# Performance work log

Hardware: AMD Instinct MI355X
Metric: run time of the kernel (lower is better)

## Reference

```python
import jax, jax.numpy as jnp
import numpy as np

B, M, S = 4, 1024, 1024
D, H, FF = 1024, 16, 4096
NE, P = 128, 1
HD = D // H
EPS = 1e-5


def _layer_norm(x, g, b):
    mu = x.mean(-1, keepdims=True)
    var = ((x - mu) ** 2).mean(-1, keepdims=True)
    return (x - mu) * jax.lax.rsqrt(var + EPS) * g + b


def _mha(q_in, kv_in, in_w, in_b, out_w, out_b):
    # torch nn.MultiheadAttention: packed in_proj_weight [3D, D], y = x @ W.T + b
    wq, wk, wv = in_w[:D], in_w[D:2 * D], in_w[2 * D:]
    bq, bk, bv = in_b[:D], in_b[D:2 * D], in_b[2 * D:]
    q = (q_in @ wq.T + bq).reshape(q_in.shape[0], q_in.shape[1], H, HD)
    k = (kv_in @ wk.T + bk).reshape(kv_in.shape[0], kv_in.shape[1], H, HD)
    v = (kv_in @ wv.T + bv).reshape(kv_in.shape[0], kv_in.shape[1], H, HD)
    scores = jnp.einsum('bqhd,bkhd->bhqk', q, k) / jnp.sqrt(jnp.float32(HD))
    attn = jax.nn.softmax(scores, axis=-1)
    o = jnp.einsum('bhqk,bkhd->bqhd', attn, v).reshape(q_in.shape[0], q_in.shape[1], D)
    return o @ out_w.T + out_b


def _soft_moe(h, phi, exp_w, exp_b):
    # h: [b, m, FF]; phi: [FF, n, p]
    logits = jnp.einsum('bmd,dnp->bmnp', h, phi)
    dispatch = jax.nn.softmax(logits, axis=1)  # over tokens m
    b, m, n, p = logits.shape
    combine = jax.nn.softmax(logits.reshape(b, m, n * p), axis=-1).reshape(b, m, n, p)
    slots = jnp.einsum('bmd,bmnp->bnpd', h, dispatch)  # [b, n, p, FF]
    y = jnp.einsum('bnpd,ndo->bnpo', slots, exp_w) + exp_b[None, :, None, :]  # [b, n, p, D]
    return jnp.einsum('bnpo,bmnp->bmo', y, combine)


def setup_inputs() -> dict:
    key = jax.random.key(0)
    ks = jax.random.split(key, 16)
    sc = 0.02

    def rn(k, shape):
        return jax.random.normal(k, shape, jnp.float32) * sc

    return {
        'tgt': jax.random.normal(ks[0], (B, M, D), jnp.float32),
        'memory': jax.random.normal(ks[1], (B, S, D), jnp.float32),
        'sa_in_w': rn(ks[2], (3 * D, D)), 'sa_in_b': jnp.zeros((3 * D,), jnp.float32),
        'sa_out_w': rn(ks[3], (D, D)), 'sa_out_b': jnp.zeros((D,), jnp.float32),
        'ca_in_w': rn(ks[4], (3 * D, D)), 'ca_in_b': jnp.zeros((3 * D,), jnp.float32),
        'ca_out_w': rn(ks[5], (D, D)), 'ca_out_b': jnp.zeros((D,), jnp.float32),
        'norm1_g': jnp.ones((D,), jnp.float32), 'norm1_b': jnp.zeros((D,), jnp.float32),
        'norm2_g': jnp.ones((D,), jnp.float32), 'norm2_b': jnp.zeros((D,), jnp.float32),
        'norm3_g': jnp.ones((D,), jnp.float32), 'norm3_b': jnp.zeros((D,), jnp.float32),
        'lin_w': rn(ks[6], (FF, D)), 'lin_b': jnp.zeros((FF,), jnp.float32),
        'phi': rn(ks[7], (FF, NE, P)),
        'exp_w': rn(ks[8], (NE, FF, D)), 'exp_b': jnp.zeros((NE, D), jnp.float32),
    }


def reference(tgt, memory, sa_in_w, sa_in_b, sa_out_w, sa_out_b,
              ca_in_w, ca_in_b, ca_out_w, ca_out_b,
              norm1_g, norm1_b, norm2_g, norm2_b, norm3_g, norm3_b,
              lin_w, lin_b, phi, exp_w, exp_b):
    # post-norm (norm_first=False), dropout=0 (eval)
    x = tgt
    x = _layer_norm(x + _mha(x, x, sa_in_w, sa_in_b, sa_out_w, sa_out_b), norm1_g, norm1_b)
    x = _layer_norm(x + _mha(x, memory, ca_in_w, ca_in_b, ca_out_w, ca_out_b), norm2_g, norm2_b)
    h = jax.nn.relu(x @ lin_w.T + lin_b)  # [B, M, FF]
    ff = _soft_moe(h, phi, exp_w, exp_b)  # [B, M, D]
    x = _layer_norm(x + ff, norm3_g, norm3_b)
    return x
```

## Files before the change

kernel.cpp:

```cpp
#include <hip/hip_runtime.h>
#include <cstdint>
#include <cstddef>

typedef unsigned short u16;
typedef unsigned int   u32;
typedef short bf16x8 __attribute__((ext_vector_type(8)));
typedef float f32x4  __attribute__((ext_vector_type(4)));
typedef u16   u16x8  __attribute__((ext_vector_type(8)));
typedef u16   u16x4  __attribute__((ext_vector_type(4)));
typedef u16   u16x2  __attribute__((ext_vector_type(2)));

constexpr int B_  = 4;
constexpr int M_  = 1024;
constexpr int S_  = 1024;
constexpr int D_  = 1024;
constexpr int H_  = 16;
constexpr int FF_ = 4096;
constexpr int NE_ = 128;

__device__ __forceinline__ u16 f2bf(float f) {
    u32 u = __builtin_bit_cast(u32, f);
    u = (u + 0x7fffu + ((u >> 16) & 1u)) >> 16;
    return (u16)u;
}
__device__ __forceinline__ float bf2f(u16 u) {
    u32 x = ((u32)u) << 16;
    return __builtin_bit_cast(float, x);
}
__device__ __forceinline__ void gload_lds16(const u16* g, u16* l) {
    __builtin_amdgcn_global_load_lds(
        (const __attribute__((address_space(1))) u32*)g,
        (__attribute__((address_space(3))) u32*)l, 16, 0, 0);
}

template<int OUT_BF16, int RELU, int HAS_BIAS>
__global__ __launch_bounds__(256) void gemm_bt_mfma(
    const u16* __restrict__ A, const u16* __restrict__ W,
    const float* __restrict__ bias, void* __restrict__ Cout,
    int K, int N, int lda, int ldw,
    size_t sA, size_t sW, size_t sC)
{
    __shared__ u16 As[128 * 32];
    __shared__ u16 Bs[128 * 32];
    const int tid = threadIdx.x;
    const int w = tid >> 6, l = tid & 63;
    const int bm = blockIdx.y * 128, bn = blockIdx.x * 128;
    const u16* Ab = A + (size_t)blockIdx.z * sA;
    const u16* Wb = W + (size_t)blockIdx.z * sW;

    const int wr = w >> 1, wc = w & 1;
    const int sr = l >> 2;
    const int sk = (l & 3) * 8;
    const u16* aG0 = Ab + (size_t)(bm + w * 16 + sr) * lda + sk;
    const u16* aG1 = Ab + (size_t)(bm + (w + 4) * 16 + sr) * lda + sk;
    const u16* bG0 = Wb + (size_t)(bn + w * 16 + sr) * ldw + sk;
    const u16* bG1 = Wb + (size_t)(bn + (w + 4) * 16 + sr) * ldw + sk;
    u16* aL0 = &As[w * 512];
    u16* aL1 = &As[(w + 4) * 512];
    u16* bL0 = &Bs[w * 512];
    u16* bL1 = &Bs[(w + 4) * 512];

    const int fr = l & 15;
    const int fk = (l >> 4) * 8;

    f32x4 acc[4][4];
#pragma unroll
    for (int i = 0; i < 4; ++i)
#pragma unroll
        for (int j = 0; j < 4; ++j)
#pragma unroll
            for (int q = 0; q < 4; ++q) acc[i][j][q] = 0.f;

    for (int k0 = 0; k0 < K; k0 += 32) {
        __syncthreads();
        gload_lds16(aG0, aL0);
        gload_lds16(aG1, aL1);
        gload_lds16(bG0, bL0);
        gload_lds16(bG1, bL1);
        aG0 += 32; aG1 += 32; bG0 += 32; bG1 += 32;
        __syncthreads();
        bf16x8 af[4], bfr[4];
#pragma unroll
        for (int m = 0; m < 4; ++m)
            af[m] = *(const bf16x8*)&As[(wr * 64 + m * 16 + fr) * 32 + fk];
#pragma unroll
        for (int n = 0; n < 4; ++n)
            bfr[n] = *(const bf16x8*)&Bs[(wc * 64 + n * 16 + fr) * 32 + fk];
#pragma unroll
        for (int m = 0; m < 4; ++m)
#pragma unroll
            for (int n = 0; n < 4; ++n)
                acc[m][n] = __builtin_amdgcn_mfma_f32_16x16x32_bf16(
                    af[m], bfr[n], acc[m][n], 0, 0, 0);
    }

    const int row0 = bm + wr * 64 + (l >> 4) * 4;
    const int col0 = bn + wc * 64;
#pragma unroll
    for (int n = 0; n < 4; ++n) {
        const int col = col0 + n * 16 + fr;
        float bv = 0.f;
        if (HAS_BIAS) bv = bias[col];
#pragma unroll
        for (int m = 0; m < 4; ++m) {
            const int row = row0 + m * 16;
#pragma unroll
            for (int j = 0; j < 4; ++j) {
                float v = acc[m][n][j] + bv;
                if (RELU) v = fmaxf(v, 0.f);
                const size_t idx = (size_t)blockIdx.z * sC + (size_t)(row + j) * N + col;
                if (OUT_BF16) ((u16*)Cout)[idx] = f2bf(v);
                else          ((float*)Cout)[idx] = v;
            }
        }
    }
}

__global__ __launch_bounds__(256) void flash_attn_kernel(
    const u16* __restrict__ Q, int qs,
    const u16* __restrict__ K, int ks,
    const u16* __restrict__ V, int vs,
    u16* __restrict__ O, int Slen)
{
    __shared__ u16 Qs[64][72];
    __shared__ u16 Ks[64][72];
    __shared__ u16 Vt[64][72];
    __shared__ u16 Pw[4][16][72];
    const int b = blockIdx.z, hh = blockIdx.y;
    const int m0 = blockIdx.x * 64;
    const int tid = threadIdx.x;
    const int w = tid >> 6, l = tid & 63;
    const int lq = l & 15, g = l >> 4;

    {
        const int row = tid >> 2, cg = (tid & 3) * 16;
        const u16* qp = Q + ((size_t)b * M_ + m0 + row) * qs + hh * 64 + cg;
        u16x8 v0 = *(const u16x8*)qp;
        u16x8 v1 = *(const u16x8*)(qp + 8);
        u16x8 o0, o1;
#pragma unroll
        for (int i = 0; i < 8; ++i) {
            o0[i] = f2bf(bf2f(v0[i]) * 0.125f);
            o1[i] = f2bf(bf2f(v1[i]) * 0.125f);
        }
        *(u16x8*)&Qs[row][cg]     = o0;
        *(u16x8*)&Qs[row][cg + 8] = o1;
    }
    __syncthreads();
    bf16x8 qf[2];
    qf[0] = *(const bf16x8*)&Qs[w * 16 + lq][g * 8];
    qf[1] = *(const bf16x8*)&Qs[w * 16 + lq][32 + g * 8];

    f32x4 acc_o[4];
#pragma unroll
    for (int nb = 0; nb < 4; ++nb)
#pragma unroll
        for (int j = 0; j < 4; ++j) acc_o[nb][j] = 0.f;
    float m_run = -1e30f, l_run = 0.f;

    const int kp = tid & 31, dg = tid >> 5;
    const int krow = tid >> 2, kcg = (tid & 3) * 16;

    for (int s0 = 0; s0 < Slen; s0 += 64) {
        __syncthreads();
        {
            const u16* kpp = K + ((size_t)b * Slen + s0 + krow) * ks + hh * 64 + kcg;
            *(u16x8*)&Ks[krow][kcg]     = *(const u16x8*)kpp;
            *(u16x8*)&Ks[krow][kcg + 8] = *(const u16x8*)(kpp + 8);
        }
        {
            const u16* vp0 = V + ((size_t)b * Slen + s0 + 2 * kp) * vs + hh * 64 + dg * 8;
            const u16* vp1 = vp0 + vs;
            u16x8 a = *(const u16x8*)vp0;
            u16x8 c = *(const u16x8*)vp1;
#pragma unroll
            for (int i = 0; i < 8; ++i) {
                u16x2 pk; pk[0] = a[i]; pk[1] = c[i];
                *(u16x2*)&Vt[dg * 8 + i][2 * kp] = pk;
            }
        }
        __syncthreads();

        f32x4 s4[4];
#pragma unroll
        for (int mb = 0; mb < 4; ++mb) {
            f32x4 z = {0.f, 0.f, 0.f, 0.f};
            bf16x8 a0 = *(const bf16x8*)&Ks[mb * 16 + lq][g * 8];
            bf16x8 a1 = *(const bf16x8*)&Ks[mb * 16 + lq][32 + g * 8];
            z = __builtin_amdgcn_mfma_f32_16x16x32_bf16(a0, qf[0], z, 0, 0, 0);
            z = __builtin_amdgcn_mfma_f32_16x16x32_bf16(a1, qf[1], z, 0, 0, 0);
            s4[mb] = z;
        }

        float pm = -1e30f;
#pragma unroll
        for (int mb = 0; mb < 4; ++mb)
#pragma unroll
            for (int j = 0; j < 4; ++j) pm = fmaxf(pm, s4[mb][j]);
        pm = fmaxf(pm, __shfl_xor(pm, 16));
        pm = fmaxf(pm, __shfl_xor(pm, 32));
        const float m_new = fmaxf(m_run, pm);
        const float alpha = __expf(m_run - m_new);
        float ls = 0.f;
        u16 pbf[4][4];
#pragma unroll
        for (int mb = 0; mb < 4; ++mb)
#pragma unroll
            for (int j = 0; j < 4; ++j) {
                float p = __expf(s4[mb][j] - m_new);
                ls += p;
                pbf[mb][j] = f2bf(p);
            }
        ls += __shfl_xor(ls, 16);
        ls += __shfl_xor(ls, 32);
        l_run = l_run * alpha + ls;
        m_run = m_new;

#pragma unroll
        for (int mb = 0; mb < 4; ++mb) {
            u16x4 pk;
            pk[0] = pbf[mb][0]; pk[1] = pbf[mb][1];
            pk[2] = pbf[mb][2]; pk[3] = pbf[mb][3];
            *(u16x4*)&Pw[w][lq][mb * 16 + g * 4] = pk;
        }

        float al[4];
#pragma unroll
        for (int j = 0; j < 4; ++j) al[j] = __shfl(alpha, 4 * g + j);
#pragma unroll
        for (int nb = 0; nb < 4; ++nb)
#pragma unroll
            for (int j = 0; j < 4; ++j) acc_o[nb][j] *= al[j];

#pragma unroll
        for (int kc = 0; kc < 2; ++kc) {
            bf16x8 pa = *(const bf16x8*)&Pw[w][lq][kc * 32 + g * 8];
#pragma unroll
            for (int nb = 0; nb < 4; ++nb) {
                bf16x8 bv = *(const bf16x8*)&Vt[nb * 16 + lq][kc * 32 + g * 8];
                acc_o[nb] = __builtin_amdgcn_mfma_f32_16x16x32_bf16(pa, bv, acc_o[nb], 0, 0, 0);
            }
        }
    }

    float linv[4];
#pragma unroll
    for (int j = 0; j < 4; ++j) linv[j] = 1.f / __shfl(l_run, 4 * g + j);
#pragma unroll
    for (int nb = 0; nb < 4; ++nb)
#pragma unroll
        for (int j = 0; j < 4; ++j) {
            const size_t row = (size_t)b * M_ + m0 + w * 16 + 4 * g + j;
            O[row * D_ + hh * 64 + nb * 16 + lq] = f2bf(acc_o[nb][j] * linv[j]);
        }
}

__global__ __launch_bounds__(256) void cvt_f32_bf16_kernel(
    const float* __restrict__ src, u16* __restrict__ dst)
{
    const size_t i = ((size_t)blockIdx.x * 256 + threadIdx.x) * 8;
    float4 a = *(const float4*)(src + i);
    float4 b = *(const float4*)(src + i + 4);
    u16x8 o;
    o[0] = f2bf(a.x); o[1] = f2bf(a.y); o[2] = f2bf(a.z); o[3] = f2bf(a.w);
    o[4] = f2bf(b.x); o[5] = f2bf(b.y); o[6] = f2bf(b.z); o[7] = f2bf(b.w);
    *(u16x8*)(dst + i) = o;
}

__global__ __launch_bounds__(256) void transpose_f32_bf16_kernel(
    const float* __restrict__ src, u16* __restrict__ dst, int R, int C,
    size_t sI, size_t sO)
{
    __shared__ u16 t[32][33];
    src += (size_t)blockIdx.z * sI;
    dst += (size_t)blockIdx.z * sO;
    const int c0 = blockIdx.x * 32, r0 = blockIdx.y * 32;
    const int x = threadIdx.x & 31, y = threadIdx.x >> 5;
    for (int i = y; i < 32; i += 8)
        t[i][x] = f2bf(src[(size_t)(r0 + i) * C + c0 + x]);
    __syncthreads();
    for (int i = y; i < 32; i += 8)
        dst[(size_t)(c0 + i) * R + r0 + x] = t[x][i];
}

__global__ __launch_bounds__(256) void transpose_bf16_kernel(
    const u16* __restrict__ src, u16* __restrict__ dst, int R, int C,
    size_t sI, size_t sO)
{
    __shared__ u16 t[32][33];
    src += (size_t)blockIdx.z * sI;
    dst += (size_t)blockIdx.z * sO;
    const int c0 = blockIdx.x * 32, r0 = blockIdx.y * 32;
    const int x = threadIdx.x & 31, y = threadIdx.x >> 5;
    for (int i = y; i < 32; i += 8)
        t[i][x] = src[(size_t)(r0 + i) * C + c0 + x];
    __syncthreads();
    for (int i = y; i < 32; i += 8)
        dst[(size_t)(c0 + i) * R + r0 + x] = t[x][i];
}

__global__ __launch_bounds__(256) void resid_ln_kernel(
    const float* __restrict__ X, const float* __restrict__ R,
    const float* __restrict__ g, const float* __restrict__ bt,
    float* __restrict__ Y, u16* __restrict__ Ybf)
{
    __shared__ float s1[4], s2[4];
    const size_t row = blockIdx.x;
    const int tid = threadIdx.x;
    const float4 x4 = *(const float4*)(X + row * 1024 + tid * 4);
    const float4 r4 = *(const float4*)(R + row * 1024 + tid * 4);
    float v[4] = {x4.x + r4.x, x4.y + r4.y, x4.z + r4.z, x4.w + r4.w};
    float s = v[0] + v[1] + v[2] + v[3];
    float q = v[0] * v[0] + v[1] * v[1] + v[2] * v[2] + v[3] * v[3];
#pragma unroll
    for (int off = 32; off; off >>= 1) {
        s += __shfl_xor(s, off);
        q += __shfl_xor(q, off);
    }
    if ((tid & 63) == 0) { s1[tid >> 6] = s; s2[tid >> 6] = q; }
    __syncthreads();
    s = s1[0] + s1[1] + s1[2] + s1[3];
    q = s2[0] + s2[1] + s2[2] + s2[3];
    const float mu = s * (1.f / 1024.f);
    const float var = q * (1.f / 1024.f) - mu * mu;
    const float rinv = rsqrtf(var + 1e-5f);
    const float4 g4 = *(const float4*)(g + tid * 4);
    const float4 b4 = *(const float4*)(bt + tid * 4);
    float o[4];
    o[0] = (v[0] - mu) * rinv * g4.x + b4.x;
    o[1] = (v[1] - mu) * rinv * g4.y + b4.y;
    o[2] = (v[2] - mu) * rinv * g4.z + b4.z;
    o[3] = (v[3] - mu) * rinv * g4.w + b4.w;
    *(float4*)(Y + row * 1024 + tid * 4) = *(float4*)o;
    if (Ybf) {
        u16x4 ob;
        ob[0] = f2bf(o[0]); ob[1] = f2bf(o[1]);
        ob[2] = f2bf(o[2]); ob[3] = f2bf(o[3]);
        *(u16x4*)(Ybf + row * 1024 + tid * 4) = ob;
    }
}

__global__ __launch_bounds__(256) void dispatch_softmax_T_kernel(
    const float* __restrict__ logitsP, u16* __restrict__ dispT)
{
    __shared__ float red[4];
    constexpr size_t CH = (size_t)B_ * M_ * NE_;
    const int n = blockIdx.x, b = blockIdx.y;
    u16* O = dispT + ((size_t)b * NE_ + n) * M_;
    const int tid = threadIdx.x;
    float v[4];
#pragma unroll
    for (int i = 0; i < 4; ++i) {
        const size_t idx = (size_t)(b * M_ + tid + 256 * i) * NE_ + n;
        v[i] = logitsP[idx] + logitsP[CH + idx] + logitsP[2 * CH + idx] + logitsP[3 * CH + idx];
    }
    float mx = fmaxf(fmaxf(v[0], v[1]), fmaxf(v[2], v[3]));
#pragma unroll
    for (int off = 32; off; off >>= 1) mx = fmaxf(mx, __shfl_xor(mx, off));
    if ((tid & 63) == 0) red[tid >> 6] = mx;
    __syncthreads();
    mx = fmaxf(fmaxf(red[0], red[1]), fmaxf(red[2], red[3]));
    __syncthreads();
    float e[4], s = 0.f;
#pragma unroll
    for (int i = 0; i < 4; ++i) { e[i] = __expf(v[i] - mx); s += e[i]; }
#pragma unroll
    for (int off = 32; off; off >>= 1) s += __shfl_xor(s, off);
    if ((tid & 63) == 0) red[tid >> 6] = s;
    __syncthreads();
    s = red[0] + red[1] + red[2] + red[3];
    const float inv = 1.f / s;
#pragma unroll
    for (int i = 0; i < 4; ++i) O[tid + 256 * i] = f2bf(e[i] * inv);
}

__global__ __launch_bounds__(64) void combine_softmax_kernel(
    const float* __restrict__ logitsP, u16* __restrict__ comb)
{
    constexpr size_t CH = (size_t)B_ * M_ * NE_;
    const size_t row = blockIdx.x;
    const int lane = threadIdx.x;
    const size_t i0 = row * NE_ + lane;
    const size_t i1 = i0 + 64;
    float a = logitsP[i0] + logitsP[CH + i0] + logitsP[2 * CH + i0] + logitsP[3 * CH + i0];
    float c = logitsP[i1] + logitsP[CH + i1] + logitsP[2 * CH + i1] + logitsP[3 * CH + i1];
    float mx = fmaxf(a, c);
#pragma unroll
    for (int off = 32; off; off >>= 1) mx = fmaxf(mx, __shfl_xor(mx, off));
    float e0 = __expf(a - mx), e1 = __expf(c - mx);
    float s = e0 + e1;
#pragma unroll
    for (int off = 32; off; off >>= 1) s += __shfl_xor(s, off);
    const float inv = 1.f / s;
    comb[row * NE_ + lane]      = f2bf(e0 * inv);
    comb[row * NE_ + lane + 64] = f2bf(e1 * inv);
}

__global__ __launch_bounds__(256) void expert_kernel(
    const float* __restrict__ slots, const float* __restrict__ exp_w,
    const float* __restrict__ exp_b, float* __restrict__ y)
{
    __shared__ float sl[4][128];
    const int n = blockIdx.x;
    const int d = blockIdx.y * 256 + threadIdx.x;
    float acc0 = 0.f, acc1 = 0.f, acc2 = 0.f, acc3 = 0.f;
    const float eb = exp_b[(size_t)n * D_ + d];
    const float* wbase = exp_w + (size_t)n * FF_ * D_ + d;
    for (int f0 = 0; f0 < FF_; f0 += 128) {
        __syncthreads();
        const int t = threadIdx.x;
        sl[t >> 7][t & 127] =
            slots[((size_t)(t >> 7) * NE_ + n) * FF_ + f0 + (t & 127)];
        sl[(t >> 7) + 2][t & 127] =
            slots[((size_t)((t >> 7) + 2) * NE_ + n) * FF_ + f0 + (t & 127)];
        __syncthreads();
        const float* wp = wbase + (size_t)f0 * D_;
#pragma unroll 8
        for (int f = 0; f < 128; ++f) {
            float w = wp[(size_t)f * D_];
            acc0 = fmaf(sl[0][f], w, acc0);
            acc1 = fmaf(sl[1][f], w, acc1);
            acc2 = fmaf(sl[2][f], w, acc2);
            acc3 = fmaf(sl[3][f], w, acc3);
        }
    }
    y[((size_t)0 * NE_ + n) * D_ + d] = acc0 + eb;
    y[((size_t)1 * NE_ + n) * D_ + d] = acc1 + eb;
    y[((size_t)2 * NE_ + n) * D_ + d] = acc2 + eb;
    y[((size_t)3 * NE_ + n) * D_ + d] = acc3 + eb;
}

extern "C" void kernel_launch(void* const* d_in, const int* in_sizes, int n_in,
                              void* d_out, int out_size, void* d_ws, size_t ws_size,
                              hipStream_t stream)
{
    const float* tgt      = (const float*)d_in[0];
    const float* memry    = (const float*)d_in[1];
    const float* sa_in_w  = (const float*)d_in[2];
    const float* sa_in_b  = (const float*)d_in[3];
    const float* sa_out_w = (const float*)d_in[4];
    const float* sa_out_b = (const float*)d_in[5];
    const float* ca_in_w  = (const float*)d_in[6];
    const float* ca_in_b  = (const float*)d_in[7];
    const float* ca_out_w = (const float*)d_in[8];
    const float* ca_out_b = (const float*)d_in[9];
    const float* norm1_g  = (const float*)d_in[10];
    const float* norm1_b  = (const float*)d_in[11];
    const float* norm2_g  = (const float*)d_in[12];
    const float* norm2_b  = (const float*)d_in[13];
    const float* norm3_g  = (const float*)d_in[14];
    const float* norm3_b  = (const float*)d_in[15];
    const float* lin_w    = (const float*)d_in[16];
    const float* lin_b    = (const float*)d_in[17];
    const float* phi      = (const float*)d_in[18];
    const float* exp_w    = (const float*)d_in[19];
    const float* exp_b    = (const float*)d_in[20];

    float* ws = (float*)d_ws;
    u16*   qkv_bf  = (u16*)(ws);
    float* proj    = ws + 6291456;
    float* x1      = ws + 10485760;
    float* x2      = ws + 14680064;
    float* logitsP = ws + 18874368;
    float* slots   = ws + 20971520;
    float* ybuf    = ws + 23068672;
    u16*   h_bf    = (u16*)(ws + 23592960);
    u16*   hT_bf   = (u16*)(ws + 31981568);
    u16*   obuf_bf = (u16*)(ws + 40370176);
    u16*   x1_bf   = (u16*)(ws + 42467328);
    u16*   x2_bf   = (u16*)(ws + 44564480);
    u16*   tgt_bf  = (u16*)(ws + 46661632);
    u16*   mem_bf  = (u16*)(ws + 48758784);
    u16*   dispT   = (u16*)(ws + 50855936);
    u16*   comb_bf = (u16*)(ws + 51118080);
    u16*   yT_bf   = (u16*)(ws + 51380224);
    u16*   w_sa_in = (u16*)(ws + 51642368);
    u16*   w_sa_out= (u16*)(ws + 53215232);
    u16*   w_ca_in = (u16*)(ws + 53739520);
    u16*   w_ca_out= (u16*)(ws + 55312384);
    u16*   w_lin   = (u16*)(ws + 55836672);
    u16*   phiT    = (u16*)(ws + 57933824);

    cvt_f32_bf16_kernel<<<2048, 256, 0, stream>>>(tgt, tgt_bf);
    cvt_f32_bf16_kernel<<<2048, 256, 0, stream>>>(memry, mem_bf);
    cvt_f32_bf16_kernel<<<1536, 256, 0, stream>>>(sa_in_w, w_sa_in);
    cvt_f32_bf16_kernel<<<512,  256, 0, stream>>>(sa_out_w, w_sa_out);
    cvt_f32_bf16_kernel<<<1536, 256, 0, stream>>>(ca_in_w, w_ca_in);
    cvt_f32_bf16_kernel<<<512,  256, 0, stream>>>(ca_out_w, w_ca_out);
    cvt_f32_bf16_kernel<<<2048, 256, 0, stream>>>(lin_w, w_lin);
    transpose_f32_bf16_kernel<<<dim3(4, 128, 1), 256, 0, stream>>>(phi, phiT, 4096, 128, 0, 0);

    gemm_bt_mfma<1, 0, 1><<<dim3(24, 32, 1), 256, 0, stream>>>(
        tgt_bf, w_sa_in, sa_in_b, qkv_bf, 1024, 3072, 1024, 1024, 0, 0, 0);
    flash_attn_kernel<<<dim3(16, 16, 4), 256, 0, stream>>>(
        qkv_bf, 3072, qkv_bf + 1024, 3072, qkv_bf + 2048, 3072, obuf_bf, S_);
    gemm_bt_mfma<0, 0, 1><<<dim3(8, 32, 1), 256, 0, stream>>>(
        obuf_bf, w_sa_out, sa_out_b, proj, 1024, 1024, 1024, 1024, 0, 0, 0);
    resid_ln_kernel<<<4096, 256, 0, stream>>>(tgt, proj, norm1_g, norm1_b, x1, x1_bf);

    u16* qca_bf = qkv_bf;
    u16* kvca_bf = qkv_bf + (size_t)4096 * 1024;
    gemm_bt_mfma<1, 0, 1><<<dim3(8, 32, 1), 256, 0, stream>>>(
        x1_bf, w_ca_in, ca_in_b, qca_bf, 1024, 1024, 1024, 1024, 0, 0, 0);
    gemm_bt_mfma<1, 0, 1><<<dim3(16, 32, 1), 256, 0, stream>>>(
        mem_bf, w_ca_in + (size_t)1024 * 1024, ca_in_b + 1024,
        kvca_bf, 1024, 2048, 1024, 1024, 0, 0, 0);
    flash_attn_kernel<<<dim3(16, 16, 4), 256, 0, stream>>>(
        qca_bf, 1024, kvca_bf, 2048, kvca_bf + 1024, 2048, obuf_bf, S_);
    gemm_bt_mfma<0, 0, 1><<<dim3(8, 32, 1), 256, 0, stream>>>(
        obuf_bf, w_ca_out, ca_out_b, proj, 1024, 1024, 1024, 1024, 0, 0, 0);
    resid_ln_kernel<<<4096, 256, 0, stream>>>(x1, proj, norm2_g, norm2_b, x2, x2_bf);

    gemm_bt_mfma<1, 1, 1><<<dim3(32, 32, 1), 256, 0, stream>>>(
        x2_bf, w_lin, lin_b, h_bf, 1024, 4096, 1024, 1024, 0, 0, 0);
    gemm_bt_mfma<0, 0, 0><<<dim3(1, 32, 4), 256, 0, stream>>>(
        h_bf, phiT, nullptr, logitsP, 1024, 128, 4096, 4096,
        1024, 1024, (size_t)B_ * M_ * NE_);
    dispatch_softmax_T_kernel<<<dim3(NE_, B_), 256, 0, stream>>>(logitsP, dispT);
    combine_softmax_kernel<<<dim3(B_ * M_), 64, 0, stream>>>(logitsP, comb_bf);
    transpose_bf16_kernel<<<dim3(128, 32, 4), 256, 0, stream>>>(
        h_bf, hT_bf, 1024, 4096, (size_t)M_ * FF_, (size_t)M_ * FF_);
    gemm_bt_mfma<0, 0, 0><<<dim3(32, 1, 4), 256, 0, stream>>>(
        dispT, hT_bf, nullptr, slots, 1024, 4096, 1024, 1024,
        (size_t)NE_ * M_, (size_t)FF_ * M_, (size_t)NE_ * FF_);
    expert_kernel<<<dim3(NE_, D_ / 256), 256, 0, stream>>>(slots, exp_w, exp_b, ybuf);
    transpose_f32_bf16_kernel<<<dim3(32, 4, 4), 256, 0, stream>>>(
        ybuf, yT_bf, 128, 1024, (size_t)NE_ * D_, (size_t)NE_ * D_);
    gemm_bt_mfma<0, 0, 0><<<dim3(8, 8, 4), 256, 0, stream>>>(
        comb_bf, yT_bf, nullptr, proj, 128, 1024, 128, 128,
        (size_t)M_ * NE_, (size_t)D_ * NE_, (size_t)M_ * D_);
    resid_ln_kernel<<<4096, 256, 0, stream>>>(x2, proj, norm3_g, norm3_b,
                                              (float*)d_out, nullptr);
}
```

Before: 896.8 us.

## Split-K expert kernel, fuse weight conversions, and lazy flash-attn rescaling

The expert matmul is rewritten as split-K over FF in 8 chunks. Each thread loads float4 weights and keeps 16 accumulators, and a separate kernel reduces the partials, adds the bias and transposes to bf16. This raises parallelism and vectorizes the 2 GB-scale fp32 weight stream. The seven f32-to-bf16 conversion launches are merged into one multi-tensor kernel to cut launch overhead. Flash attention skips the running-max update and accumulator rescale while the new block max stays within 8 of the running max, at some risk to bf16 precision of P.

```diff
diff --git a/kernel.cpp b/kernel.cpp
--- a/kernel.cpp
+++ b/kernel.cpp
@@ -199,22 +199,44 @@
             for (int j = 0; j < 4; ++j) pm = fmaxf(pm, s4[mb][j]);
         pm = fmaxf(pm, __shfl_xor(pm, 16));
         pm = fmaxf(pm, __shfl_xor(pm, 32));
-        const float m_new = fmaxf(m_run, pm);
-        const float alpha = __expf(m_run - m_new);
+
+        u16 pbf[4][4];
         float ls = 0.f;
-        u16 pbf[4][4];
-#pragma unroll
-        for (int mb = 0; mb < 4; ++mb)
-#pragma unroll
-            for (int j = 0; j < 4; ++j) {
-                float p = __expf(s4[mb][j] - m_new);
-                ls += p;
-                pbf[mb][j] = f2bf(p);
-            }
-        ls += __shfl_xor(ls, 16);
-        ls += __shfl_xor(ls, 32);
-        l_run = l_run * alpha + ls;
-        m_run = m_new;
+        if (__all(pm - m_run <= 8.f)) {
+#pragma unroll
+            for (int mb = 0; mb < 4; ++mb)
+#pragma unroll
+                for (int j = 0; j < 4; ++j) {
+                    float p = __expf(s4[mb][j] - m_run);
+                    ls += p;
+                    pbf[mb][j] = f2bf(p);
+                }
+            ls += __shfl_xor(ls, 16);
+            ls += __shfl_xor(ls, 32);
+            l_run += ls;
+        } else {
+            const float m_new = fmaxf(m_run, pm);
+            const float alpha = __expf(m_run - m_new);
+#pragma unroll
+            for (int mb = 0; mb < 4; ++mb)
+#pragma unroll
+                for (int j = 0; j < 4; ++j) {
+                    float p = __expf(s4[mb][j] - m_new);
+                    ls += p;
+                    pbf[mb][j] = f2bf(p);
+                }
+            ls += __shfl_xor(ls, 16);
+            ls += __shfl_xor(ls, 32);
+            l_run = l_run * alpha + ls;
+            m_run = m_new;
+            float al[4];
+#pragma unroll
+            for (int j = 0; j < 4; ++j) al[j] = __shfl(alpha, 4 * g + j);
+#pragma unroll
+            for (int nb = 0; nb < 4; ++nb)
+#pragma unroll
+                for (int j = 0; j < 4; ++j) acc_o[nb][j] *= al[j];
+        }
 
 #pragma unroll
         for (int mb = 0; mb < 4; ++mb) {
@@ -224,14 +246,6 @@
             *(u16x4*)&Pw[w][lq][mb * 16 + g * 4] = pk;
         }
 
-        float al[4];
-#pragma unroll
-        for (int j = 0; j < 4; ++j) al[j] = __shfl(alpha, 4 * g + j);
-#pragma unroll
-        for (int nb = 0; nb < 4; ++nb)
-#pragma unroll
-            for (int j = 0; j < 4; ++j) acc_o[nb][j] *= al[j];
-
 #pragma unroll
         for (int kc = 0; kc < 2; ++kc) {
             bf16x8 pa = *(const bf16x8*)&Pw[w][lq][kc * 32 + g * 8];
@@ -255,16 +269,31 @@
         }
 }
 
-__global__ __launch_bounds__(256) void cvt_f32_bf16_kernel(
-    const float* __restrict__ src, u16* __restrict__ dst)
-{
-    const size_t i = ((size_t)blockIdx.x * 256 + threadIdx.x) * 8;
-    float4 a = *(const float4*)(src + i);
-    float4 b = *(const float4*)(src + i + 4);
+__global__ __launch_bounds__(256) void cvt_multi_kernel(
+    const float* __restrict__ s0, u16* __restrict__ d0,
+    const float* __restrict__ s1, u16* __restrict__ d1,
+    const float* __restrict__ s2, u16* __restrict__ d2,
+    const float* __restrict__ s3, u16* __restrict__ d3,
+    const float* __restrict__ s4, u16* __restrict__ d4,
+    const float* __restrict__ s5, u16* __restrict__ d5,
+    const float* __restrict__ s6, u16* __restrict__ d6)
+{
+    int blk = blockIdx.x;
+    const float* s; u16* d;
+    if      (blk < 2048) { s = s0; d = d0; }
+    else if (blk < 4096) { s = s1; d = d1; blk -= 2048; }
+    else if (blk < 5632) { s = s2; d = d2; blk -= 4096; }
+    else if (blk < 6144) { s = s3; d = d3; blk -= 5632; }
+    else if (blk < 7680) { s = s4; d = d4; blk -= 6144; }
+    else if (blk < 8192) { s = s5; d = d5; blk -= 7680; }
+    else                 { s = s6; d = d6; blk -= 8192; }
+    const size_t i = ((size_t)blk * 256 + threadIdx.x) * 8;
+    float4 a = *(const float4*)(s + i);
+    float4 b = *(const float4*)(s + i + 4);
     u16x8 o;
     o[0] = f2bf(a.x); o[1] = f2bf(a.y); o[2] = f2bf(a.z); o[3] = f2bf(a.w);
     o[4] = f2bf(b.x); o[5] = f2bf(b.y); o[6] = f2bf(b.z); o[7] = f2bf(b.w);
-    *(u16x8*)(dst + i) = o;
+    *(u16x8*)(d + i) = o;
 }
 
 __global__ __launch_bounds__(256) void transpose_f32_bf16_kernel(
@@ -396,38 +425,63 @@
     comb[row * NE_ + lane + 64] = f2bf(e1 * inv);
 }
 
-__global__ __launch_bounds__(256) void expert_kernel(
+__global__ __launch_bounds__(256) void expert_partial_kernel(
     const float* __restrict__ slots, const float* __restrict__ exp_w,
-    const float* __restrict__ exp_b, float* __restrict__ y)
-{
-    __shared__ float sl[4][128];
+    float* __restrict__ part)
+{
+    __shared__ float sl[4][512];
     const int n = blockIdx.x;
-    const int d = blockIdx.y * 256 + threadIdx.x;
-    float acc0 = 0.f, acc1 = 0.f, acc2 = 0.f, acc3 = 0.f;
-    const float eb = exp_b[(size_t)n * D_ + d];
-    const float* wbase = exp_w + (size_t)n * FF_ * D_ + d;
-    for (int f0 = 0; f0 < FF_; f0 += 128) {
-        __syncthreads();
-        const int t = threadIdx.x;
-        sl[t >> 7][t & 127] =
-            slots[((size_t)(t >> 7) * NE_ + n) * FF_ + f0 + (t & 127)];
-        sl[(t >> 7) + 2][t & 127] =
-            slots[((size_t)((t >> 7) + 2) * NE_ + n) * FF_ + f0 + (t & 127)];
-        __syncthreads();
-        const float* wp = wbase + (size_t)f0 * D_;
-#pragma unroll 8
-        for (int f = 0; f < 128; ++f) {
-            float w = wp[(size_t)f * D_];
-            acc0 = fmaf(sl[0][f], w, acc0);
-            acc1 = fmaf(sl[1][f], w, acc1);
-            acc2 = fmaf(sl[2][f], w, acc2);
-            acc3 = fmaf(sl[3][f], w, acc3);
-        }
-    }
-    y[((size_t)0 * NE_ + n) * D_ + d] = acc0 + eb;
-    y[((size_t)1 * NE_ + n) * D_ + d] = acc1 + eb;
-    y[((size_t)2 * NE_ + n) * D_ + d] = acc2 + eb;
-    y[((size_t)3 * NE_ + n) * D_ + d] = acc3 + eb;
+    const int c = blockIdx.y;
+    const int f0 = c * 512;
+    const int t = threadIdx.x;
+    for (int i = t; i < 2048; i += 256) {
+        const int b = i >> 9, f = i & 511;
+        sl[b][f] = slots[((size_t)b * NE_ + n) * FF_ + f0 + f];
+    }
+    __syncthreads();
+    const int d4 = t * 4;
+    const float* wp = exp_w + ((size_t)n * FF_ + f0) * D_ + d4;
+    f32x4 acc[4];
+#pragma unroll
+    for (int b = 0; b < 4; ++b)
+#pragma unroll
+        for (int j = 0; j < 4; ++j) acc[b][j] = 0.f;
+#pragma unroll 4
+    for (int f = 0; f < 512; ++f) {
+        const float4 w4 = *(const float4*)wp;
+        wp += D_;
+#pragma unroll
+        for (int b = 0; b < 4; ++b) {
+            const float s = sl[b][f];
+            acc[b][0] = fmaf(s, w4.x, acc[b][0]);
+            acc[b][1] = fmaf(s, w4.y, acc[b][1]);
+            acc[b][2] = fmaf(s, w4.z, acc[b][2]);
+            acc[b][3] = fmaf(s, w4.w, acc[b][3]);
+        }
+    }
+#pragma unroll
+    for (int b = 0; b < 4; ++b)
+        *(f32x4*)&part[(((size_t)c * 4 + b) * NE_ + n) * D_ + d4] = acc[b];
+}
+
+__global__ __launch_bounds__(256) void reduce_yT_kernel(
+    const float* __restrict__ part, const float* __restrict__ exp_b,
+    u16* __restrict__ yT)
+{
+    __shared__ float tile[32][33];
+    const int d0 = blockIdx.x * 32, n0 = blockIdx.y * 32, b = blockIdx.z;
+    const int x = threadIdx.x & 31, y = threadIdx.x >> 5;
+    for (int i = y; i < 32; i += 8) {
+        const int n = n0 + i;
+        float s = exp_b[(size_t)n * D_ + d0 + x];
+#pragma unroll
+        for (int c = 0; c < 8; ++c)
+            s += part[(((size_t)c * 4 + b) * NE_ + n) * D_ + d0 + x];
+        tile[i][x] = s;
+    }
+    __syncthreads();
+    for (int i = y; i < 32; i += 8)
+        yT[((size_t)b * D_ + d0 + i) * NE_ + n0 + x] = f2bf(tile[x][i]);
 }
 
 extern "C" void kernel_launch(void* const* d_in, const int* in_sizes, int n_in,
@@ -462,32 +516,29 @@
     float* x1      = ws + 10485760;
     float* x2      = ws + 14680064;
     float* logitsP = ws + 18874368;
-    float* slots   = ws + 20971520;
-    float* ybuf    = ws + 23068672;
-    u16*   h_bf    = (u16*)(ws + 23592960);
-    u16*   hT_bf   = (u16*)(ws + 31981568);
-    u16*   obuf_bf = (u16*)(ws + 40370176);
-    u16*   x1_bf   = (u16*)(ws + 42467328);
-    u16*   x2_bf   = (u16*)(ws + 44564480);
-    u16*   tgt_bf  = (u16*)(ws + 46661632);
-    u16*   mem_bf  = (u16*)(ws + 48758784);
-    u16*   dispT   = (u16*)(ws + 50855936);
-    u16*   comb_bf = (u16*)(ws + 51118080);
-    u16*   yT_bf   = (u16*)(ws + 51380224);
-    u16*   w_sa_in = (u16*)(ws + 51642368);
-    u16*   w_sa_out= (u16*)(ws + 53215232);
-    u16*   w_ca_in = (u16*)(ws + 53739520);
-    u16*   w_ca_out= (u16*)(ws + 55312384);
-    u16*   w_lin   = (u16*)(ws + 55836672);
-    u16*   phiT    = (u16*)(ws + 57933824);
-
-    cvt_f32_bf16_kernel<<<2048, 256, 0, stream>>>(tgt, tgt_bf);
-    cvt_f32_bf16_kernel<<<2048, 256, 0, stream>>>(memry, mem_bf);
-    cvt_f32_bf16_kernel<<<1536, 256, 0, stream>>>(sa_in_w, w_sa_in);
-    cvt_f32_bf16_kernel<<<512,  256, 0, stream>>>(sa_out_w, w_sa_out);
-    cvt_f32_bf16_kernel<<<1536, 256, 0, stream>>>(ca_in_w, w_ca_in);
-    cvt_f32_bf16_kernel<<<512,  256, 0, stream>>>(ca_out_w, w_ca_out);
-    cvt_f32_bf16_kernel<<<2048, 256, 0, stream>>>(lin_w, w_lin);
+    float* part    = ws + 20971520;
+    u16*   h_bf    = (u16*)(ws + 25165824);
+    u16*   hT_bf   = (u16*)(ws + 33554432);
+    u16*   obuf_bf = (u16*)(ws + 41943040);
+    u16*   x1_bf   = (u16*)(ws + 44040192);
+    u16*   x2_bf   = (u16*)(ws + 46137344);
+    u16*   tgt_bf  = (u16*)(ws + 48234496);
+    u16*   mem_bf  = (u16*)(ws + 50331648);
+    u16*   dispT   = (u16*)(ws + 52428800);
+    u16*   comb_bf = (u16*)(ws + 52690944);
+    u16*   yT_bf   = (u16*)(ws + 52953088);
+    u16*   slots_n = 0; float* slots = ws + 53215232;
+    (void)slots_n;
+    u16*   w_sa_in = (u16*)(ws + 55312384);
+    u16*   w_sa_out= (u16*)(ws + 56885248);
+    u16*   w_ca_in = (u16*)(ws + 57409536);
+    u16*   w_ca_out= (u16*)(ws + 58982400);
+    u16*   w_lin   = (u16*)(ws + 59506688);
+    u16*   phiT    = (u16*)(ws + 61603840);
+
+    cvt_multi_kernel<<<10240, 256, 0, stream>>>(
+        tgt, tgt_bf, memry, mem_bf, sa_in_w, w_sa_in, sa_out_w, w_sa_out,
+        ca_in_w, w_ca_in, ca_out_w, w_ca_out, lin_w, w_lin);
     transpose_f32_bf16_kernel<<<dim3(4, 128, 1), 256, 0, stream>>>(phi, phiT, 4096, 128, 0, 0);
 
     gemm_bt_mfma<1, 0, 1><<<dim3(24, 32, 1), 256, 0, stream>>>(
@@ -523,9 +574,8 @@
     gemm_bt_mfma<0, 0, 0><<<dim3(32, 1, 4), 256, 0, stream>>>(
         dispT, hT_bf, nullptr, slots, 1024, 4096, 1024, 1024,
         (size_t)NE_ * M_, (size_t)FF_ * M_, (size_t)NE_ * FF_);
-    expert_kernel<<<dim3(NE_, D_ / 256), 256, 0, stream>>>(slots, exp_w, exp_b, ybuf);
-    transpose_f32_bf16_kernel<<<dim3(32, 4, 4), 256, 0, stream>>>(
-        ybuf, yT_bf, 128, 1024, (size_t)NE_ * D_, (size_t)NE_ * D_);
+    expert_partial_kernel<<<dim3(NE_, 8), 256, 0, stream>>>(slots, exp_w, part);
+    reduce_yT_kernel<<<dim3(32, 4, 4), 256, 0, stream>>>(part, exp_b, yT_bf);
     gemm_bt_mfma<0, 0, 0><<<dim3(8, 8, 4), 256, 0, stream>>>(
         comb_bf, yT_bf, nullptr, proj, 128, 1024, 128, 128,
         (size_t)M_ * NE_, (size_t)D_ * NE_, (size_t)M_ * D_);
```

Result: faster. 839.0 us (-6.4%).
